# Kernel optimization log

Hardware: AMD Instinct MI355X
Metric: run time of the kernel (lower is better)

Reference implementation:

```python
import jax, jax.numpy as jnp
import numpy as np

P, D, NF, NR, ND, EF, ER = 512, 128, 50000, 50000, 100000, 400000, 400000
BASELINE = 6.0


def setup_inputs() -> dict:
    key = jax.random.key(0)
    ctr = [0]
    def nk():
        ctr[0] += 1
        return jax.random.fold_in(key, ctr[0])
    def nrm(shape, scale=1.0):
        return jax.random.normal(nk(), shape, dtype=jnp.float32) * scale
    def uni(shape):
        return jax.random.uniform(nk(), shape, dtype=jnp.float32)
    def lin(fi, fo):
        return nrm((fi, fo), fi ** -0.5), jnp.zeros((fo,), jnp.float32)
    inp = {}
    inp['target_features'] = nrm((P,))
    inp['form_features'] = nrm((NF, P))
    inp['role_features'] = nrm((NR, P))
    inp['form_binds_y'] = BASELINE + nrm((EF,))
    inp['form_binds_w'] = uni((EF,))
    inp['role_binds_y'] = BASELINE + nrm((ER,))
    inp['role_binds_w'] = uni((ER,))
    inp['form_diff_w'] = uni((NF,)) + 0.01
    inp['role_diff_w'] = uni((NR,)) + 0.01
    inp['trust_vector'] = uni((3,))
    inp['drug_features'] = nrm((ND, D))
    inp['form_w1'], inp['form_b1'] = lin(P, P); inp['form_a1'] = jnp.full((1,), 0.25, jnp.float32)
    inp['form_w2'], inp['form_b2'] = lin(P, P)
    inp['role_w1'], inp['role_b1'] = lin(P, P); inp['role_a1'] = jnp.full((1,), 0.25, jnp.float32)
    inp['role_w2'], inp['role_b2'] = lin(P, P)
    inp['q_w'], inp['q_b'] = lin(P, D)
    inp['k_w'], inp['k_b'] = lin(D, D)
    inp['v_w'], inp['v_b'] = lin(D, D)
    inp['layer_emb'] = nrm((2, 16))
    inp['attn_w1'], inp['attn_b1'] = lin(2 * P + 16, 128)
    inp['attn_w2'], inp['attn_b2'] = lin(128, 64)
    inp['attn_w3'], inp['attn_b3'] = lin(64, 1)
    inp['mix_w1'], inp['mix_b1'] = lin(2 * D + 3, 64); inp['mix_a'] = jnp.full((1,), 0.25, jnp.float32)
    inp['mix_w2'], inp['mix_b2'] = lin(64, 2)
    inp['int_w1'], inp['int_b1'] = lin(D, P); inp['int_a'] = jnp.full((1,), 0.25, jnp.float32)
    inp['int_w2'], inp['int_b2'] = lin(P, P)
    inp['norm_w'] = jnp.ones((P,), jnp.float32)
    inp['norm_b'] = jnp.zeros((P,), jnp.float32)
    inp['delta_gate'] = jnp.float32(0.5)
    inp['form_neighbors'] = jnp.arange(NF, dtype=jnp.int32)
    inp['role_neighbors'] = jnp.arange(NR, dtype=jnp.int32)
    inp['form_binds_src'] = jax.random.randint(nk(), (EF,), 0, NF, dtype=jnp.int32)
    inp['form_binds_dst'] = jax.random.randint(nk(), (EF,), 0, ND, dtype=jnp.int32)
    inp['role_binds_src'] = jax.random.randint(nk(), (ER,), 0, NR, dtype=jnp.int32)
    inp['role_binds_dst'] = jax.random.randint(nk(), (ER,), 0, ND, dtype=jnp.int32)
    return inp


def _prelu(x, a):
    return jnp.where(x >= 0, x, a * x)


def _mlp2(x, w1, b1, a, w2, b2):
    return _prelu(x @ w1 + b1, a) @ w2 + b2


def _ln(x, w=None, b=None, eps=1e-5):
    m = jnp.mean(x, -1, keepdims=True)
    v = jnp.mean((x - m) ** 2, -1, keepdims=True)
    y = (x - m) * jax.lax.rsqrt(v + eps)
    return y if w is None else y * w + b


def _pref(z, nid, src, dst, y, w, drugs, q_w, q_b, k_w, k_b, v_w, v_b):
    # segment-softmax attention over (neighbor protein -> drug) bipartite edges
    N = nid.shape[0]
    order = jnp.argsort(nid)
    s = nid[order]
    pos = jnp.searchsorted(s, src)
    clip = jnp.minimum(pos, N - 1)
    valid = (pos < N) & (s[clip] == src)
    seg = jnp.where(valid, order[clip], N)  # invalid edges -> dump segment N
    q = z @ q_w + q_b                       # [D]
    d = drugs[dst]                          # [E, D] gather
    k = d @ k_w + k_b
    v = (d @ v_w + v_b) * ((y - BASELINE) * w)[:, None]
    logits = (k @ q) / (k.shape[-1] ** 0.5)
    mx = jax.ops.segment_max(logits, seg, num_segments=N + 1)
    mx = jnp.where(jnp.isfinite(mx), mx, 0.0)
    ex = jnp.where(valid, jnp.exp(logits - mx[seg]), 0.0)
    den = jax.ops.segment_sum(ex, seg, num_segments=N + 1) + 1e-12
    attn = ex / den[seg]
    return jax.ops.segment_sum(v * attn[:, None], seg, num_segments=N + 1)[:N]


def _attn_logits(z, zn, lemb, w1, b1, w2, b2, w3, b3):
    N = zn.shape[0]
    x = jnp.concatenate([jnp.broadcast_to(z, (N, z.shape[0])), zn,
                         jnp.broadcast_to(lemb, (N, lemb.shape[0]))], axis=-1)
    h = jax.nn.leaky_relu(x @ w1 + b1, 0.2)
    h = jax.nn.leaky_relu(h @ w2 + b2, 0.2)
    return (h @ w3 + b3)[:, 0]


def _core(fl, form_neighbors, role_neighbors, form_binds_src, form_binds_dst, role_binds_src, role_binds_dst):
    (target_features, form_features, role_features, form_binds_y, form_binds_w,
     role_binds_y, role_binds_w, form_diff_w, role_diff_w, trust_vector, drug_features,
     form_w1, form_b1, form_a1, form_w2, form_b2,
     role_w1, role_b1, role_a1, role_w2, role_b2,
     q_w, q_b, k_w, k_b, v_w, v_b, layer_emb,
     attn_w1, attn_b1, attn_w2, attn_b2, attn_w3, attn_b3,
     mix_w1, mix_b1, mix_a, mix_w2, mix_b2,
     int_w1, int_b1, int_a, int_w2, int_b2,
     norm_w, norm_b, delta_gate) = fl
    z_form = _mlp2(target_features, form_w1, form_b1, form_a1, form_w2, form_b2)
    z_role = _mlp2(target_features, role_w1, role_b1, role_a1, role_w2, role_b2)
    z = 0.5 * (z_form + z_role)
    form_feats = _mlp2(form_features, form_w1, form_b1, form_a1, form_w2, form_b2)
    role_feats = _mlp2(role_features, role_w1, role_b1, role_a1, role_w2, role_b2)
    form_msgs = _pref(z, form_neighbors, form_binds_src, form_binds_dst, form_binds_y, form_binds_w, drug_features, q_w, q_b, k_w, k_b, v_w, v_b)
    role_msgs = _pref(z, role_neighbors, role_binds_src, role_binds_dst, role_binds_y, role_binds_w, drug_features, q_w, q_b, k_w, k_b, v_w, v_b)
    form_logits = _attn_logits(z, form_feats, layer_emb[0], attn_w1, attn_b1, attn_w2, attn_b2, attn_w3, attn_b3)
    role_logits = _attn_logits(z, role_feats, layer_emb[1], attn_w1, attn_b1, attn_w2, attn_b2, attn_w3, attn_b3)
    form_attn = jax.nn.softmax(form_logits + jnp.log(jnp.maximum(form_diff_w, 1e-12)))
    role_attn = jax.nn.softmax(role_logits + jnp.log(jnp.maximum(role_diff_w, 1e-12)))
    v_form = form_attn @ form_msgs
    v_role = role_attn @ role_msgs
    mixer_in = jnp.concatenate([v_form, v_role, trust_vector])
    lw = jax.nn.softmax(_mlp2(mixer_in, mix_w1, mix_b1, mix_a, mix_w2, mix_b2))
    w_form, w_role = lw[0], lw[1]
    v_prior = w_form * v_form + w_role * v_role
    form_delta = form_attn @ (z[None, :] - form_feats)
    role_delta = role_attn @ (z[None, :] - role_feats)
    delta_raw = w_form * form_delta + w_role * role_delta
    delta_mean = delta_gate * _ln(delta_raw)
    z_refined = _ln(z + _mlp2(v_prior, int_w1, int_b1, int_a, int_w2, int_b2), norm_w, norm_b)
    return z_refined, v_prior, delta_mean


def reference(target_features, form_features, role_features, form_binds_y, form_binds_w, role_binds_y, role_binds_w, form_diff_w, role_diff_w, trust_vector, drug_features, form_w1, form_b1, form_a1, form_w2, form_b2, role_w1, role_b1, role_a1, role_w2, role_b2, q_w, q_b, k_w, k_b, v_w, v_b, layer_emb, attn_w1, attn_b1, attn_w2, attn_b2, attn_w3, attn_b3, mix_w1, mix_b1, mix_a, mix_w2, mix_b2, int_w1, int_b1, int_a, int_w2, int_b2, norm_w, norm_b, delta_gate, form_neighbors, role_neighbors, form_binds_src, form_binds_dst, role_binds_src, role_binds_dst):
    fl = (target_features, form_features, role_features, form_binds_y, form_binds_w,
          role_binds_y, role_binds_w, form_diff_w, role_diff_w, trust_vector, drug_features,
          form_w1, form_b1, form_a1, form_w2, form_b2,
          role_w1, role_b1, role_a1, role_w2, role_b2,
          q_w, q_b, k_w, k_b, v_w, v_b, layer_emb,
          attn_w1, attn_b1, attn_w2, attn_b2, attn_w3, attn_b3,
          mix_w1, mix_b1, mix_a, mix_w2, mix_b2,
          int_w1, int_b1, int_a, int_w2, int_b2,
          norm_w, norm_b, delta_gate)
    return _core(fl, form_neighbors, role_neighbors, form_binds_src, form_binds_dst, role_binds_src, role_binds_dst)
```

## Files before the change

### kernel.cpp

```cpp
#include <hip/hip_runtime.h>

#define NFN 50000
#define NDR 100000
#define NE  400000
#define MT  391
#define M0PAD 50048

__device__ __forceinline__ float bf2f(unsigned short u) {
    return __uint_as_float(((unsigned)u) << 16);
}
__device__ __forceinline__ unsigned short f2bf(float f) {
    unsigned u = __float_as_uint(f);
    unsigned r = 0x7FFFu + ((u >> 16) & 1u);
    return (unsigned short)((u + r) >> 16);
}
__device__ __forceinline__ unsigned bpack(float lo, float hi) {
    return (__float_as_uint(hi) & 0xFFFF0000u) | (__float_as_uint(lo) >> 16);
}

typedef __attribute__((ext_vector_type(8))) short bf16x8;
typedef __attribute__((ext_vector_type(4))) float f32x4;

struct KArgs {
    const float *tf, *ff, *rf, *fby, *fbw, *rby, *rbw, *fdw, *rdw, *trust, *drugs;
    const float *fw1, *fb1, *fa1, *fw2, *fb2, *rw1, *rb1, *ra1, *rw2, *rb2;
    const float *qw, *qb, *kw, *kb, *vw, *vb, *lemb;
    const float *aw1, *ab1, *aw2, *ab2, *aw3, *ab3;
    const float *mw1, *mb1, *ma, *mw2, *mb2;
    const float *iw1, *ib1, *ia, *iw2, *ib2;
    const float *nw, *nb, *dgate;
    const int *fsrc, *fdst, *rsrc, *rdst;
    float *shf, *shr;
    float *svf, *svr;
    float *gdenf, *gdenr;
    float *edenf, *edenr;
    float *cdf, *cdr;
    float *hraw;
    float *zraw;
    float *qraw;
    float *b1f, *b1r;
    float *sfr;
    float *o2raw;
    float *qk, *c0, *pe;
    unsigned short *w1tf, *w1tr;
    unsigned short *w2atf, *w2atr;
    unsigned short *aw2t;
    float *nexf, *nexr;
    unsigned short *H;
    float *hi;
    float *wfwr;
    float *out;
};

__global__ __launch_bounds__(512) void kA(KArgs A) {
    const int b = blockIdx.x;
    const int side = b >> 5, chunk = b & 31;
    const int tt = threadIdx.x;
    const float* w1 = side ? A.rw1 : A.fw1;
    float acc = 0.f;
    const int i0 = chunk * 16;
#pragma unroll
    for (int k = 0; k < 16; k++) {
        int i = i0 + k;
        acc = fmaf(A.tf[i], w1[(size_t)i * 512 + tt], acc);
    }
    atomicAdd(&A.hraw[side * 512 + tt], acc);
}

__global__ __launch_bounds__(512) void kB(KArgs A) {
    const int b = blockIdx.x;
    const int side = b >> 4, chunk = b & 15;
    const int tt = threadIdx.x;
    const float* w2 = side ? A.rw2 : A.fw2;
    const float* b1 = side ? A.rb1 : A.fb1;
    const float aa = (side ? A.ra1 : A.fa1)[0];
    float acc = 0.f;
    const int i0 = chunk * 32;
    for (int k = 0; k < 32; k++) {
        int i = i0 + k;
        float h = A.hraw[side * 512 + i] + b1[i];
        h = h >= 0.f ? h : aa * h;
        acc = fmaf(h, w2[(size_t)i * 512 + tt], acc);
    }
    if (b == 0) acc += A.fb2[tt] + A.rb2[tt];
    atomicAdd(&A.zraw[tt], acc);
}

__global__ __launch_bounds__(512) void kC1(KArgs A) {
    const int b = blockIdx.x;
    const int t = threadIdx.x;
    const int j = t & 127, isub = t >> 7;
    if (b < 8) {
        const int i0 = b * 64 + isub * 16;
        float acc = 0.f;
        for (int k = 0; k < 16; k++) {
            int i = i0 + k;
            acc = fmaf(0.5f * A.zraw[i], A.qw[(size_t)i * 128 + j], acc);
        }
        atomicAdd(&A.qraw[j], acc);
        if (b == 0 && t < 128) atomicAdd(&A.qraw[t], A.qb[t]);
    } else if (b < 16) {
        const int chunk = b - 8;
        const int i0 = chunk * 64 + isub * 16;
        float acc = 0.f;
        for (int k = 0; k < 16; k++) {
            int i = i0 + k;
            acc = fmaf(0.5f * A.zraw[i], A.aw1[(size_t)i * 128 + j], acc);
            acc = fmaf(A.fb2[i], A.aw1[(size_t)(512 + i) * 128 + j], acc);
        }
        atomicAdd(&A.b1f[j], acc);
        if (b == 8 && t < 128) {
            float c = A.ab1[t];
            for (int l = 0; l < 16; l++) c = fmaf(A.lemb[l], A.aw1[(size_t)(1024 + l) * 128 + t], c);
            atomicAdd(&A.b1f[t], c);
        }
    } else {
        const int chunk = b - 16;
        const int i0 = chunk * 64 + isub * 16;
        float acc = 0.f;
        for (int k = 0; k < 16; k++) {
            int i = i0 + k;
            acc = fmaf(0.5f * A.zraw[i], A.aw1[(size_t)i * 128 + j], acc);
            acc = fmaf(A.rb2[i], A.aw1[(size_t)(512 + i) * 128 + j], acc);
        }
        atomicAdd(&A.b1r[j], acc);
        if (b == 16 && t < 128) {
            float c = A.ab1[t];
            for (int l = 0; l < 16; l++) c = fmaf(A.lemb[16 + l], A.aw1[(size_t)(1024 + l) * 128 + t], c);
            atomicAdd(&A.b1r[t], c);
        }
    }
}

__global__ __launch_bounds__(256) void kC2(KArgs A) {
    const int t = threadIdx.x;
    __shared__ float sq[128];
    if (t < 128) sq[t] = A.qraw[t];
    __syncthreads();
    if (t < 128) {
        float s = 0.f;
        for (int j = 0; j < 128; j++) s = fmaf(A.kw[t * 128 + j], sq[j], s);
        A.qk[t] = s;
    } else if (t == 128) {
        float c = 0.f;
        for (int j = 0; j < 128; j++) c = fmaf(A.kb[j], sq[j], c);
        A.c0[0] = c;
    }
}

__global__ __launch_bounds__(512) void k_prep(KArgs A) {
    const int b = blockIdx.x;
    const int t = threadIdx.x;
    if (b < 128) {
        __shared__ float tl[64][65];
        const int side = b >> 6, tile = b & 63;
        const int k0 = (tile >> 3) * 64, n0 = (tile & 7) * 64;
        const float* w1 = side ? A.rw1 : A.fw1;
        unsigned short* o = side ? A.w1tr : A.w1tf;
        const int col = t & 63, rg = t >> 6;
#pragma unroll
        for (int i = 0; i < 8; i++) {
            const int row = rg * 8 + i;
            tl[row][col] = w1[(size_t)(k0 + row) * 512 + n0 + col];
        }
        __syncthreads();
#pragma unroll
        for (int i = 0; i < 8; i++) {
            const int nrow = rg * 8 + i;
            o[(size_t)(n0 + nrow) * 512 + k0 + col] = f2bf(tl[col][nrow]);
        }
    } else if (b < 384) {
        const int lb = b - 128;
        const int side = lb >> 7;
        const int i = (lb & 127) * 4 + (t >> 7);
        const int j = t & 127;
        const float* w2 = side ? A.rw2 : A.fw2;
        unsigned short* outp = side ? A.w2atr : A.w2atf;
        float s = 0.f;
        for (int k = 0; k < 512; k++)
            s = fmaf(w2[i * 512 + k], A.aw1[(size_t)(512 + k) * 128 + j], s);
        outp[(size_t)j * 512 + i] = f2bf(s);
    } else if (b < 400) {
        const int elem = (b - 384) * 512 + t;
        const int j = elem >> 7, i = elem & 127;
        A.aw2t[j * 128 + i] = f2bf(A.aw2[i * 64 + j]);
    } else {
        const int lane = t & 63;
        const int w = (b - 400) * 8 + (t >> 6);
        const float2 qk2 = *(const float2*)(A.qk + 2 * lane);
        const float c0 = A.c0[0];
        for (int dr = w; dr < NDR; dr += 2048) {
            float2 dv = *(const float2*)(A.drugs + (size_t)dr * 128 + 2 * lane);
            float p = fmaf(dv.x, qk2.x, dv.y * qk2.y);
            for (int off = 32; off >= 1; off >>= 1) p += __shfl_xor(p, off, 64);
            if (lane == 0) A.pe[dr] = expf((p + c0) * 0.088388347648318447f);
        }
    }
}

__global__ __launch_bounds__(256, 2)
void mfma_gemm(KArgs A) {
    __shared__ __align__(16) float Afb[2][128 * 32];
    __shared__ __align__(16) unsigned short Bbuf[2][128 * 32];
    const int t = threadIdx.x;
    const int lane = t & 63, wv = t >> 6;
    const int p = blockIdx.x;
    const int L = (p & 7) * MT + (p >> 3);
    const int side = L >= (MT * 4);
    const int lbid = L - side * (MT * 4);
    const int m0l = (lbid >> 2) * 128, n0 = (lbid & 3) * 128;
    const float* __restrict__ Xf = side ? A.rf : A.ff;
    const unsigned short* __restrict__ Bt = side ? A.w1tr : A.w1tf;
    const float* __restrict__ bias = side ? A.rb1 : A.fb1;
    const float aval = (side ? A.ra1 : A.fa1)[0];
    unsigned short* __restrict__ Cv = A.H + (size_t)side * M0PAD * 512;
    const int wm = (wv >> 1) * 64, wn = (wv & 1) * 64;
    const int lm = lane & 15, ko = lane >> 4;
    const int K = 512;

    f32x4 acc[4][4];
#pragma unroll
    for (int i = 0; i < 4; i++)
#pragma unroll
        for (int j = 0; j < 4; j++) acc[i][j] = (f32x4){0.f, 0.f, 0.f, 0.f};

    auto stage = [&](int buf, int k0) {
#pragma unroll
        for (int ii = 0; ii < 4; ii++) {
            const int inst = wv * 4 + ii;
            const int rl = inst * 8 + (lane >> 3);
            const int sl = (lane & 7) ^ (rl & 7);
            int ar = m0l + rl; if (ar >= NFN) ar = NFN - 1;
            __builtin_amdgcn_global_load_lds(
                (const __attribute__((address_space(1))) void*)(Xf + (size_t)ar * K + k0 + sl * 4),
                (__attribute__((address_space(3))) void*)(&Afb[buf][inst * 256]), 16, 0, 0);
        }
#pragma unroll
        for (int ii = 0; ii < 2; ii++) {
            const int inst = wv * 2 + ii;
            const int rl = inst * 16 + (lane >> 2);
            const int sl = (lane & 3) ^ ((rl >> 1) & 3);
            __builtin_amdgcn_global_load_lds(
                (const __attribute__((address_space(1))) void*)(Bt + (size_t)(n0 + rl) * K + k0 + sl * 8),
                (__attribute__((address_space(3))) void*)(&Bbuf[buf][inst * 512]), 16, 0, 0);
        }
    };

    auto compute = [&](int buf) {
        bf16x8 af[4], bfr[4];
#pragma unroll
        for (int mi = 0; mi < 4; mi++) {
            int row = wm + mi * 16 + lm;
            int s0 = (ko * 2) ^ (row & 7);
            int s1 = (ko * 2 + 1) ^ (row & 7);
            f32x4 fa = *(const f32x4*)&Afb[buf][row * 32 + s0 * 4];
            f32x4 fb = *(const f32x4*)&Afb[buf][row * 32 + s1 * 4];
            unsigned u0 = bpack(fa[0], fa[1]);
            unsigned u1 = bpack(fa[2], fa[3]);
            unsigned u2 = bpack(fb[0], fb[1]);
            unsigned u3 = bpack(fb[2], fb[3]);
            uint4 uu = make_uint4(u0, u1, u2, u3);
            af[mi] = *(bf16x8*)&uu;
        }
#pragma unroll
        for (int ni = 0; ni < 4; ni++) {
            int col = wn + ni * 16 + lm;
            bfr[ni] = *(const bf16x8*)&Bbuf[buf][col * 32 + ((ko ^ ((col >> 1) & 3)) * 8)];
        }
#pragma unroll
        for (int mi = 0; mi < 4; mi++)
#pragma unroll
            for (int ni = 0; ni < 4; ni++)
                acc[mi][ni] = __builtin_amdgcn_mfma_f32_16x16x32_bf16(af[mi], bfr[ni], acc[mi][ni], 0, 0, 0);
    };

    stage(0, 0);
    __syncthreads();
    for (int kt = 0; kt < 16; kt++) {
        if (kt + 1 < 16) stage((kt + 1) & 1, (kt + 1) * 32);
        compute(kt & 1);
        __syncthreads();
    }

#pragma unroll
    for (int mi = 0; mi < 4; mi++) {
#pragma unroll
        for (int reg = 0; reg < 4; reg++) {
            int row = m0l + wm + mi * 16 + ko * 4 + reg;
#pragma unroll
            for (int ni = 0; ni < 4; ni++) {
                int col = n0 + wn + ni * 16 + lm;
                float v = acc[mi][ni][reg] + bias[col];
                v = v >= 0.f ? v : aval * v;
                Cv[(size_t)row * 512 + col] = f2bf(v);
            }
        }
    }
}

__global__ __launch_bounds__(256, 2)
void gemm_logits(KArgs A) {
    __shared__ __align__(16) unsigned short Abuf[2][128 * 32];
    __shared__ __align__(16) unsigned short Bbuf[2][128 * 32];
    __shared__ __align__(16) unsigned short Gs[128][136];
    __shared__ float ps[128];
    __shared__ float red2[128];
    __shared__ float snex[128];
    const int bid = blockIdx.x;
    const int side = bid >= MT;
    const int m0l = (bid - side * MT) * 128;
    const unsigned short* __restrict__ Ab = A.H + (size_t)side * M0PAD * 512;
    const unsigned short* __restrict__ Bt = side ? A.w2atr : A.w2atf;
    const float* __restrict__ bias = side ? A.b1r : A.b1f;
    const float* __restrict__ dw = side ? A.rdw : A.fdw;
    float* __restrict__ nex = side ? A.nexr : A.nexf;
    float* __restrict__ gden = side ? A.gdenr : A.gdenf;
    const int t = threadIdx.x;
    const int lane = t & 63, wv = t >> 6;
    const int wm = (wv >> 1) * 64, wn = (wv & 1) * 64;
    const int lm = lane & 15, ko = lane >> 4;
    const int K = 512;

    f32x4 acc[4][4];
#pragma unroll
    for (int i = 0; i < 4; i++)
#pragma unroll
        for (int j = 0; j < 4; j++) acc[i][j] = (f32x4){0.f, 0.f, 0.f, 0.f};

    auto stage = [&](int buf, int k0) {
#pragma unroll
        for (int ii = 0; ii < 2; ii++) {
            const int inst = wv * 2 + ii;
            const int rl = inst * 16 + (lane >> 2);
            const int sl = (lane & 3) ^ ((rl >> 1) & 3);
            int ar = m0l + rl; if (ar >= NFN) ar = NFN - 1;
            __builtin_amdgcn_global_load_lds(
                (const __attribute__((address_space(1))) void*)(Ab + (size_t)ar * K + k0 + sl * 8),
                (__attribute__((address_space(3))) void*)(&Abuf[buf][inst * 512]), 16, 0, 0);
            __builtin_amdgcn_global_load_lds(
                (const __attribute__((address_space(1))) void*)(Bt + (size_t)rl * K + k0 + sl * 8),
                (__attribute__((address_space(3))) void*)(&Bbuf[buf][inst * 512]), 16, 0, 0);
        }
    };

    auto compute = [&](int buf) {
        bf16x8 af[4], bfr[4];
#pragma unroll
        for (int mi = 0; mi < 4; mi++) {
            int row = wm + mi * 16 + lm;
            af[mi] = *(const bf16x8*)&Abuf[buf][row * 32 + ((ko ^ ((row >> 1) & 3)) * 8)];
        }
#pragma unroll
        for (int ni = 0; ni < 4; ni++) {
            int col = wn + ni * 16 + lm;
            bfr[ni] = *(const bf16x8*)&Bbuf[buf][col * 32 + ((ko ^ ((col >> 1) & 3)) * 8)];
        }
#pragma unroll
        for (int mi = 0; mi < 4; mi++)
#pragma unroll
            for (int ni = 0; ni < 4; ni++)
                acc[mi][ni] = __builtin_amdgcn_mfma_f32_16x16x32_bf16(af[mi], bfr[ni], acc[mi][ni], 0, 0, 0);
    };

    stage(0, 0);
    __syncthreads();
    for (int kt = 0; kt < 16; kt++) {
        if (kt + 1 < 16) stage((kt + 1) & 1, (kt + 1) * 32);
        compute(kt & 1);
        __syncthreads();
    }

#pragma unroll
    for (int mi = 0; mi < 4; mi++) {
#pragma unroll
        for (int reg = 0; reg < 4; reg++) {
            int row_l = wm + mi * 16 + ko * 4 + reg;
#pragma unroll
            for (int ni = 0; ni < 4; ni++) {
                int col = wn + ni * 16 + lm;
                float v = acc[mi][ni][reg] + bias[col];
                v = v >= 0.f ? v : 0.2f * v;
                Gs[row_l][col] = f2bf(v);
            }
        }
    }
    __syncthreads();

    const int wr0 = wv * 32;
    float ab2v[4], aw3v[4];
#pragma unroll
    for (int ni = 0; ni < 4; ni++) {
        int col = ni * 16 + lm;
        ab2v[ni] = A.ab2[col];
        aw3v[ni] = A.aw3[col];
    }
    f32x4 acc2[2][4];
#pragma unroll
    for (int i = 0; i < 2; i++)
#pragma unroll
        for (int j = 0; j < 4; j++) acc2[i][j] = (f32x4){0.f, 0.f, 0.f, 0.f};
#pragma unroll
    for (int kk = 0; kk < 4; kk++) {
        bf16x8 ga[2], bb[4];
#pragma unroll
        for (int mi = 0; mi < 2; mi++)
            ga[mi] = *(const bf16x8*)&Gs[wr0 + mi * 16 + lm][kk * 32 + ko * 8];
#pragma unroll
        for (int ni = 0; ni < 4; ni++)
            bb[ni] = *(const bf16x8*)(A.aw2t + (size_t)(ni * 16 + lm) * 128 + kk * 32 + ko * 8);
#pragma unroll
        for (int mi = 0; mi < 2; mi++)
#pragma unroll
            for (int ni = 0; ni < 4; ni++)
                acc2[mi][ni] = __builtin_amdgcn_mfma_f32_16x16x32_bf16(ga[mi], bb[ni], acc2[mi][ni], 0, 0, 0);
    }
#pragma unroll
    for (int mi = 0; mi < 2; mi++) {
#pragma unroll
        for (int reg = 0; reg < 4; reg++) {
            float s = 0.f;
#pragma unroll
            for (int ni = 0; ni < 4; ni++) {
                float v = acc2[mi][ni][reg] + ab2v[ni];
                v = v >= 0.f ? v : 0.2f * v;
                s = fmaf(v, aw3v[ni], s);
            }
            s += __shfl_xor(s, 1, 64);
            s += __shfl_xor(s, 2, 64);
            s += __shfl_xor(s, 4, 64);
            s += __shfl_xor(s, 8, 64);
            if (lm == 0) ps[wr0 + mi * 16 + ko * 4 + reg] = s;
        }
    }
    __syncthreads();
    float val = 0.f;
    if (t < 128) {
        int node = m0l + t;
        if (node < NFN) {
            val = expf(ps[t] + A.ab3[0] + logf(fmaxf(dw[node], 1e-12f)));
            nex[node] = val;
        }
        snex[t] = val;
        red2[t] = val;
    }
    __syncthreads();
    if (t < 64) red2[t] += red2[t + 64];
    __syncthreads();
    if (t < 32) red2[t] += red2[t + 32];
    __syncthreads();
    if (t < 16) red2[t] += red2[t + 16];
    __syncthreads();
    if (t == 0) {
        float s = 0.f;
        for (int i = 0; i < 16; i++) s += red2[i];
        atomicAdd(gden, s);
    }
    {
        const unsigned short* Hrow = Ab + (size_t)m0l * 512;
        float a0 = 0.f, a1 = 0.f;
        for (int r = 0; r < 128; r += 2) {
            const float w0 = snex[r], w1 = snex[r + 1];
            const unsigned v0 = *(const unsigned*)(Hrow + (size_t)r * 512 + 2 * t);
            const unsigned v1 = *(const unsigned*)(Hrow + (size_t)(r + 1) * 512 + 2 * t);
            a0 = fmaf(w0, bf2f((unsigned short)(v0 & 0xFFFFu)), a0);
            a1 = fmaf(w0, bf2f((unsigned short)(v0 >> 16)), a1);
            a0 = fmaf(w1, bf2f((unsigned short)(v1 & 0xFFFFu)), a0);
            a1 = fmaf(w1, bf2f((unsigned short)(v1 >> 16)), a1);
        }
        float* SH = side ? A.shr : A.shf;
        atomicAdd(&SH[2 * t], a0);
        atomicAdd(&SH[2 * t + 1], a1);
    }
}

__global__ __launch_bounds__(256) void k_edge1(KArgs A) {
    const int side = blockIdx.y;
    const int* src = side ? A.rsrc : A.fsrc;
    const int* dst = side ? A.rdst : A.fdst;
    float* eden = side ? A.edenr : A.edenf;
    const int base = blockIdx.x * 2048 + threadIdx.x;
#pragma unroll
    for (int u = 0; u < 8; u++) {
        const int e = base + u * 256;
        if (e < NE) atomicAdd(&eden[src[e]], A.pe[dst[e]]);
    }
}

__global__ __launch_bounds__(256) void k_nfac(KArgs A) {
    const int side = blockIdx.y;
    const int n = blockIdx.x * 256 + threadIdx.x;
    if (n >= NFN) return;
    const float* nex = side ? A.nexr : A.nexf;
    float* eden = side ? A.edenr : A.edenf;
    const float invden = 1.0f / *(side ? A.gdenr : A.gdenf);
    eden[n] = nex[n] * invden / (eden[n] + 1e-12f);
}

__global__ __launch_bounds__(256) void k_edge2(KArgs A) {
    const int side = blockIdx.y;
    const int* src = side ? A.rsrc : A.fsrc;
    const int* dst = side ? A.rdst : A.fdst;
    const float* yy = side ? A.rby : A.fby;
    const float* ww = side ? A.rbw : A.fbw;
    const float* fac = side ? A.edenr : A.edenf;
    float* cd = side ? A.cdr : A.cdf;
    float* sv = side ? A.svr : A.svf;
    const int base = blockIdx.x * 2048 + threadIdx.x;
    float csum = 0.f;
#pragma unroll
    for (int u = 0; u < 8; u++) {
        const int e = base + u * 256;
        if (e < NE) {
            float coef = fac[src[e]] * A.pe[dst[e]] * ((yy[e] - 6.0f) * ww[e]);
            atomicAdd(&cd[dst[e]], coef);
            csum += coef;
        }
    }
    __shared__ float red[256];
    red[threadIdx.x] = csum; __syncthreads();
    for (int s2 = 128; s2 >= 1; s2 >>= 1) {
        if (threadIdx.x < s2) red[threadIdx.x] += red[threadIdx.x + s2];
        __syncthreads();
    }
    if (threadIdx.x == 0) atomicAdd(&sv[128], red[0]);
}

__global__ __launch_bounds__(256) void k_wsumD(KArgs A) {
    const int t = threadIdx.x;
    const int col = t & 127, rg = t >> 7;
    __shared__ float red[2][2][128];
    float af = 0.f, ar = 0.f;
    for (int dr = blockIdx.x * 2 + rg; dr < NDR; dr += gridDim.x * 2) {
        float cf = A.cdf[dr], cr = A.cdr[dr];
        float dv = A.drugs[(size_t)dr * 128 + col];
        af = fmaf(cf, dv, af);
        ar = fmaf(cr, dv, ar);
    }
    red[rg][0][col] = af; red[rg][1][col] = ar;
    __syncthreads();
    if (rg == 0) {
        atomicAdd(&A.svf[col], red[0][0][col] + red[1][0][col]);
        atomicAdd(&A.svr[col], red[0][1][col] + red[1][1][col]);
    }
}

__global__ __launch_bounds__(512) void kF12(KArgs A) {
    const int b = blockIdx.x;
    const int t = threadIdx.x;
    if (b < 16) {
        const int side = b >> 3, chunk = b & 7;
        const float* w2 = side ? A.rw2 : A.fw2;
        const float* SH = side ? A.shr : A.shf;
        const float invden = 1.0f / *(side ? A.gdenr : A.gdenf);
        float acc = 0.f;
        const int i0 = chunk * 64;
        for (int k = 0; k < 64; k++) {
            int i = i0 + k;
            acc = fmaf(SH[i], w2[(size_t)i * 512 + t], acc);
        }
        acc *= invden;
        if (chunk == 0) acc += (side ? A.rb2 : A.fb2)[t];
        atomicAdd(&A.sfr[side * 512 + t], acc);
        return;
    }
    __shared__ float vform[128], vrole[128], vprior[128], mh[64], sw[2];
    if (t < 128) {
        float vf = A.svf[128] * A.vb[t];
        float vr = A.svr[128] * A.vb[t];
        for (int i = 0; i < 128; i++) {
            vf = fmaf(A.svf[i], A.vw[i * 128 + t], vf);
            vr = fmaf(A.svr[i], A.vw[i * 128 + t], vr);
        }
        vform[t] = vf; vrole[t] = vr;
    }
    __syncthreads();
    if (t < 64) {
        float m = A.mb1[t];
        for (int i = 0; i < 128; i++) m = fmaf(vform[i], A.mw1[i * 64 + t], m);
        for (int i = 0; i < 128; i++) m = fmaf(vrole[i], A.mw1[(128 + i) * 64 + t], m);
        for (int i = 0; i < 3; i++)   m = fmaf(A.trust[i], A.mw1[(256 + i) * 64 + t], m);
        float ma = A.ma[0];
        mh[t] = m >= 0.f ? m : ma * m;
    }
    __syncthreads();
    if (t < 2) {
        float o = A.mb2[t];
        for (int i = 0; i < 64; i++) o = fmaf(mh[i], A.mw2[i * 2 + t], o);
        sw[t] = o;
    }
    __syncthreads();
    const float mo = fmaxf(sw[0], sw[1]);
    const float e0 = expf(sw[0] - mo), e1 = expf(sw[1] - mo);
    const float wf = e0 / (e0 + e1), wr = e1 / (e0 + e1);
    if (t == 0) { A.wfwr[0] = wf; A.wfwr[1] = wr; }
    if (t < 128) {
        float vp = wf * vform[t] + wr * vrole[t];
        vprior[t] = vp;
        A.out[512 + t] = vp;
    }
    __syncthreads();
    float hi = A.ib1[t];
    for (int i = 0; i < 128; i++) hi = fmaf(vprior[i], A.iw1[(size_t)i * 512 + t], hi);
    float ia = A.ia[0];
    A.hi[t] = hi >= 0.f ? hi : ia * hi;
}

__global__ __launch_bounds__(512) void kF3(KArgs A) {
    const int chunk = blockIdx.x;
    const int tt = threadIdx.x;
    float acc = 0.f;
    const int i0 = chunk * 64;
    for (int k = 0; k < 64; k++) {
        int i = i0 + k;
        acc = fmaf(A.hi[i], A.iw2[(size_t)i * 512 + tt], acc);
    }
    if (chunk == 0) acc += A.ib2[tt];
    atomicAdd(&A.o2raw[tt], acc);
}

__global__ __launch_bounds__(512) void kF4(KArgs A) {
    const int t = threadIdx.x;
    __shared__ float red[512];
    const float wf = A.wfwr[0], wr = A.wfwr[1];
    const float zv = 0.5f * A.zraw[t];
    float dr_ = zv - wf * A.sfr[t] - wr * A.sfr[512 + t];
    red[t] = dr_; __syncthreads();
    for (int s = 256; s >= 1; s >>= 1) { if (t < s) red[t] += red[t + s]; __syncthreads(); }
    float mean = red[0] * (1.f / 512.f); __syncthreads();
    float dd = dr_ - mean;
    red[t] = dd * dd; __syncthreads();
    for (int s = 256; s >= 1; s >>= 1) { if (t < s) red[t] += red[t + s]; __syncthreads(); }
    float var = red[0] * (1.f / 512.f); __syncthreads();
    A.out[640 + t] = A.dgate[0] * (dd * rsqrtf(var + 1e-5f));
    float zin = zv + A.o2raw[t];
    red[t] = zin; __syncthreads();
    for (int s = 256; s >= 1; s >>= 1) { if (t < s) red[t] += red[t + s]; __syncthreads(); }
    float mean2 = red[0] * (1.f / 512.f); __syncthreads();
    float d2 = zin - mean2;
    red[t] = d2 * d2; __syncthreads();
    for (int s = 256; s >= 1; s >>= 1) { if (t < s) red[t] += red[t + s]; __syncthreads(); }
    float var2 = red[0] * (1.f / 512.f);
    A.out[t] = (d2 * rsqrtf(var2 + 1e-5f)) * A.nw[t] + A.nb[t];
}

extern "C" void kernel_launch(void* const* d_in, const int* in_sizes, int n_in,
                              void* d_out, int out_size, void* d_ws, size_t ws_size,
                              hipStream_t stream) {
    (void)in_sizes; (void)n_in; (void)out_size;
    KArgs A;
    A.tf    = (const float*)d_in[0];
    A.ff    = (const float*)d_in[1];
    A.rf    = (const float*)d_in[2];
    A.fby   = (const float*)d_in[3];
    A.fbw   = (const float*)d_in[4];
    A.rby   = (const float*)d_in[5];
    A.rbw   = (const float*)d_in[6];
    A.fdw   = (const float*)d_in[7];
    A.rdw   = (const float*)d_in[8];
    A.trust = (const float*)d_in[9];
    A.drugs = (const float*)d_in[10];
    A.fw1 = (const float*)d_in[11]; A.fb1 = (const float*)d_in[12]; A.fa1 = (const float*)d_in[13];
    A.fw2 = (const float*)d_in[14]; A.fb2 = (const float*)d_in[15];
    A.rw1 = (const float*)d_in[16]; A.rb1 = (const float*)d_in[17]; A.ra1 = (const float*)d_in[18];
    A.rw2 = (const float*)d_in[19]; A.rb2 = (const float*)d_in[20];
    A.qw = (const float*)d_in[21]; A.qb = (const float*)d_in[22];
    A.kw = (const float*)d_in[23]; A.kb = (const float*)d_in[24];
    A.vw = (const float*)d_in[25]; A.vb = (const float*)d_in[26];
    A.lemb = (const float*)d_in[27];
    A.aw1 = (const float*)d_in[28]; A.ab1 = (const float*)d_in[29];
    A.aw2 = (const float*)d_in[30]; A.ab2 = (const float*)d_in[31];
    A.aw3 = (const float*)d_in[32]; A.ab3 = (const float*)d_in[33];
    A.mw1 = (const float*)d_in[34]; A.mb1 = (const float*)d_in[35]; A.ma = (const float*)d_in[36];
    A.mw2 = (const float*)d_in[37]; A.mb2 = (const float*)d_in[38];
    A.iw1 = (const float*)d_in[39]; A.ib1 = (const float*)d_in[40]; A.ia = (const float*)d_in[41];
    A.iw2 = (const float*)d_in[42]; A.ib2 = (const float*)d_in[43];
    A.nw = (const float*)d_in[44]; A.nb = (const float*)d_in[45];
    A.dgate = (const float*)d_in[46];
    A.fsrc = (const int*)d_in[49];
    A.fdst = (const int*)d_in[50];
    A.rsrc = (const int*)d_in[51];
    A.rdst = (const int*)d_in[52];
    A.out = (float*)d_out;

    char* w = (char*)d_ws;
    size_t off = 0;
    auto alloc = [&](size_t bytes) -> void* {
        void* p = w + off;
        off = (off + bytes + 255) & ~(size_t)255;
        return p;
    };
    A.shf   = (float*)alloc(512 * 4);
    A.shr   = (float*)alloc(512 * 4);
    A.svf   = (float*)alloc(129 * 4);
    A.svr   = (float*)alloc(129 * 4);
    A.gdenf = (float*)alloc(4);
    A.gdenr = (float*)alloc(4);
    A.edenf = (float*)alloc((size_t)NFN * 4);
    A.edenr = (float*)alloc((size_t)NFN * 4);
    A.cdf   = (float*)alloc((size_t)NDR * 4);
    A.cdr   = (float*)alloc((size_t)NDR * 4);
    A.hraw  = (float*)alloc(1024 * 4);
    A.zraw  = (float*)alloc(512 * 4);
    A.qraw  = (float*)alloc(128 * 4);
    A.b1f   = (float*)alloc(128 * 4);
    A.b1r   = (float*)alloc(128 * 4);
    A.sfr   = (float*)alloc(1024 * 4);
    A.o2raw = (float*)alloc(512 * 4);
    const size_t zbytes = off;
    A.qk   = (float*)alloc(128 * 4);
    A.c0   = (float*)alloc(4);
    A.pe   = (float*)alloc((size_t)NDR * 4);
    A.w1tf = (unsigned short*)alloc((size_t)512 * 512 * 2);
    A.w1tr = (unsigned short*)alloc((size_t)512 * 512 * 2);
    A.w2atf = (unsigned short*)alloc((size_t)128 * 512 * 2);
    A.w2atr = (unsigned short*)alloc((size_t)128 * 512 * 2);
    A.aw2t  = (unsigned short*)alloc((size_t)64 * 128 * 2);
    A.nexf  = (float*)alloc((size_t)NFN * 4);
    A.nexr  = (float*)alloc((size_t)NFN * 4);
    A.H     = (unsigned short*)alloc((size_t)2 * M0PAD * 512 * 2);
    A.hi    = (float*)alloc(512 * 4);
    A.wfwr  = (float*)alloc(2 * 4);
    if (ws_size && off > ws_size) return;

    hipMemsetAsync(d_ws, 0, zbytes, stream);

    kA<<<64, 512, 0, stream>>>(A);
    kB<<<32, 512, 0, stream>>>(A);
    kC1<<<24, 512, 0, stream>>>(A);
    kC2<<<1, 256, 0, stream>>>(A);
    k_prep<<<656, 512, 0, stream>>>(A);

    const int EB8 = (NE + 2047) / 2048;
    const int NFB = (NFN + 255) / 256;
    mfma_gemm<<<2 * MT * 4, 256, 0, stream>>>(A);
    gemm_logits<<<2 * MT, 256, 0, stream>>>(A);
    k_edge1<<<dim3(EB8, 2), 256, 0, stream>>>(A);
    k_nfac<<<dim3(NFB, 2), 256, 0, stream>>>(A);
    k_edge2<<<dim3(EB8, 2), 256, 0, stream>>>(A);
    k_wsumD<<<512, 256, 0, stream>>>(A);
    kF12<<<17, 512, 0, stream>>>(A);
    kF3<<<8, 512, 0, stream>>>(A);
    kF4<<<1, 512, 0, stream>>>(A);
}
```

Before: 451.1 us.

## Convert A tile to bf16 once during staging via registers instead of per-wave

New measurement: 435.6 us. 1.04x faster.

```diff
diff --git a/kernel.cpp b/kernel.cpp
--- a/kernel.cpp
+++ b/kernel.cpp
@@ -200,7 +200,7 @@
 
 __global__ __launch_bounds__(256, 2)
 void mfma_gemm(KArgs A) {
-    __shared__ __align__(16) float Afb[2][128 * 32];
+    __shared__ __align__(16) unsigned short Ab16[2][128 * 32];
     __shared__ __align__(16) unsigned short Bbuf[2][128 * 32];
     const int t = threadIdx.x;
     const int lane = t & 63, wv = t >> 6;
@@ -218,23 +218,38 @@
     const int lm = lane & 15, ko = lane >> 4;
     const int K = 512;
 
+    const int row0 = t >> 2, oct0 = t & 3;
+    int ar0 = m0l + row0;       if (ar0 >= NFN) ar0 = NFN - 1;
+    int ar1 = m0l + 64 + row0;  if (ar1 >= NFN) ar1 = NFN - 1;
+    const float* __restrict__ asrc0 = Xf + (size_t)ar0 * K + oct0 * 8;
+    const float* __restrict__ asrc1 = Xf + (size_t)ar1 * K + oct0 * 8;
+    const int aslot0 = oct0 ^ ((row0 >> 1) & 3);
+    const int aslot1 = oct0 ^ (((row0 + 64) >> 1) & 3);
+    unsigned short* const adst0 = &(((unsigned short*)Ab16)[0]) ;
+
     f32x4 acc[4][4];
 #pragma unroll
     for (int i = 0; i < 4; i++)
 #pragma unroll
         for (int j = 0; j < 4; j++) acc[i][j] = (f32x4){0.f, 0.f, 0.f, 0.f};
 
-    auto stage = [&](int buf, int k0) {
-#pragma unroll
-        for (int ii = 0; ii < 4; ii++) {
-            const int inst = wv * 4 + ii;
-            const int rl = inst * 8 + (lane >> 3);
-            const int sl = (lane & 7) ^ (rl & 7);
-            int ar = m0l + rl; if (ar >= NFN) ar = NFN - 1;
-            __builtin_amdgcn_global_load_lds(
-                (const __attribute__((address_space(1))) void*)(Xf + (size_t)ar * K + k0 + sl * 4),
-                (__attribute__((address_space(3))) void*)(&Afb[buf][inst * 256]), 16, 0, 0);
-        }
+    f32x4 rg[4];
+
+    auto aload = [&](int k0) {
+        rg[0] = *(const f32x4*)(asrc0 + k0);
+        rg[1] = *(const f32x4*)(asrc0 + k0 + 4);
+        rg[2] = *(const f32x4*)(asrc1 + k0);
+        rg[3] = *(const f32x4*)(asrc1 + k0 + 4);
+    };
+    auto awrite = [&](int buf) {
+        uint4 w0 = make_uint4(bpack(rg[0][0], rg[0][1]), bpack(rg[0][2], rg[0][3]),
+                              bpack(rg[1][0], rg[1][1]), bpack(rg[1][2], rg[1][3]));
+        uint4 w1 = make_uint4(bpack(rg[2][0], rg[2][1]), bpack(rg[2][2], rg[2][3]),
+                              bpack(rg[3][0], rg[3][1]), bpack(rg[3][2], rg[3][3]));
+        *(uint4*)&Ab16[buf][row0 * 32 + aslot0 * 8] = w0;
+        *(uint4*)&Ab16[buf][(row0 + 64) * 32 + aslot1 * 8] = w1;
+    };
+    auto stageB = [&](int buf, int k0) {
 #pragma unroll
         for (int ii = 0; ii < 2; ii++) {
             const int inst = wv * 2 + ii;
@@ -251,16 +266,7 @@
 #pragma unroll
         for (int mi = 0; mi < 4; mi++) {
             int row = wm + mi * 16 + lm;
-            int s0 = (ko * 2) ^ (row & 7);
-            int s1 = (ko * 2 + 1) ^ (row & 7);
-            f32x4 fa = *(const f32x4*)&Afb[buf][row * 32 + s0 * 4];
-            f32x4 fb = *(const f32x4*)&Afb[buf][row * 32 + s1 * 4];
-            unsigned u0 = bpack(fa[0], fa[1]);
-            unsigned u1 = bpack(fa[2], fa[3]);
-            unsigned u2 = bpack(fb[0], fb[1]);
-            unsigned u3 = bpack(fb[2], fb[3]);
-            uint4 uu = make_uint4(u0, u1, u2, u3);
-            af[mi] = *(bf16x8*)&uu;
+            af[mi] = *(const bf16x8*)&Ab16[buf][row * 32 + ((ko ^ ((row >> 1) & 3)) * 8)];
         }
 #pragma unroll
         for (int ni = 0; ni < 4; ni++) {
@@ -274,11 +280,18 @@
                 acc[mi][ni] = __builtin_amdgcn_mfma_f32_16x16x32_bf16(af[mi], bfr[ni], acc[mi][ni], 0, 0, 0);
     };
 
-    stage(0, 0);
+    aload(0);
+    stageB(0, 0);
+    awrite(0);
     __syncthreads();
     for (int kt = 0; kt < 16; kt++) {
-        if (kt + 1 < 16) stage((kt + 1) & 1, (kt + 1) * 32);
-        compute(kt & 1);
+        const int cur = kt & 1, nxt = cur ^ 1;
+        if (kt + 1 < 16) {
+            aload((kt + 1) * 32);
+            stageB(nxt, (kt + 1) * 32);
+        }
+        compute(cur);
+        if (kt + 1 < 16) awrite(nxt);
         __syncthreads();
     }
 
```
